# Kernel tuning notes

Hardware: AMD Instinct MI355X
Metric: run time of the kernel (lower is better)

Reference implementation:

```python
import jax, jax.numpy as jnp
import numpy as np

N = 1_000_000
F_IN = 16
HID = 32
E = 16_000_000


def setup_inputs() -> dict:
    key = jax.random.key(0)
    ks = jax.random.split(key, 20)
    s = 0.1
    inp = {
        "x": jax.random.normal(ks[0], (N, F_IN), dtype=jnp.float32),
        "edge_index": jax.random.randint(ks[1], (2, E), 0, N, dtype=jnp.int64),
        "edge_weight": jax.random.uniform(ks[2], (E,), dtype=jnp.float32),
        # ChebConv(K=1) weights for the 3 GRU gates (x-side and h-side)
        "Wxz": jax.random.normal(ks[3], (F_IN, HID), dtype=jnp.float32) * s,
        "bxz": jnp.zeros((HID,), jnp.float32),
        "Whz": jax.random.normal(ks[4], (HID, HID), dtype=jnp.float32) * s,
        "bhz": jnp.zeros((HID,), jnp.float32),
        "Wxr": jax.random.normal(ks[5], (F_IN, HID), dtype=jnp.float32) * s,
        "bxr": jnp.zeros((HID,), jnp.float32),
        "Whr": jax.random.normal(ks[6], (HID, HID), dtype=jnp.float32) * s,
        "bhr": jnp.zeros((HID,), jnp.float32),
        "Wxh": jax.random.normal(ks[7], (F_IN, HID), dtype=jnp.float32) * s,
        "bxh": jnp.zeros((HID,), jnp.float32),
        "Whh": jax.random.normal(ks[8], (HID, HID), dtype=jnp.float32) * s,
        "bhh": jnp.zeros((HID,), jnp.float32),
        # final Linear(32, 1)
        "Wlin": jax.random.normal(ks[9], (HID, 1), dtype=jnp.float32) * s,
        "blin": jnp.zeros((1,), jnp.float32),
    }
    return inp


def _gconv_gru(x, Wxz, bxz, Whz, bhz, Wxr, bxr, Whr, bhr, Wxh, bxh, Whh, bhh):
    # GConvGRU with ChebConv K=1: each conv is T0(L)x @ W + b == x @ W + b
    # (edge_index / edge_weight are mathematically unused when K=1).
    H = jnp.zeros((x.shape[0], Whz.shape[0]), dtype=x.dtype)  # initial hidden state
    Z = jax.nn.sigmoid(x @ Wxz + bxz + H @ Whz + bhz)          # update gate
    R = jax.nn.sigmoid(x @ Wxr + bxr + H @ Whr + bhr)          # reset gate
    H_tilde = jnp.tanh(x @ Wxh + bxh + (R * H) @ Whh + bhh)    # candidate
    return Z * H + (1.0 - Z) * H_tilde


def reference(x, edge_index, edge_weight, Wxz, bxz, Whz, bhz, Wxr, bxr, Whr, bhr,
              Wxh, bxh, Whh, bhh, Wlin, blin):
    H = _gconv_gru(x, Wxz, bxz, Whz, bhz, Wxr, bxr, Whr, bhr, Wxh, bxh, Whh, bhh)
    h = jax.nn.relu(H)
    return h @ Wlin + blin  # [N, 1]
```

## Files before the change

kernel.cpp:

```cpp
#include <hip/hip_runtime.h>


typedef float v2f __attribute__((ext_vector_type(2)));

constexpr int F   = 16;
constexpr int HD  = 32;
constexpr int NPT = 4;
constexpr int JB  = 4;

__global__ __launch_bounds__(256) void gru_fused(
    const float* __restrict__ x,
    const float* __restrict__ Wxz, const float* __restrict__ bxz,
    const float* __restrict__ bhz,
    const float* __restrict__ Wxh, const float* __restrict__ bxh,
    const float* __restrict__ bhh,
    const float* __restrict__ Wlin, const float* __restrict__ blin,
    float* __restrict__ out, int n)
{
    const int t = blockIdx.x * 256 + threadIdx.x;
    const int base = t * NPT;
    if (base >= n) return;

    float xs[NPT][F];
    #pragma unroll
    for (int m = 0; m < NPT; ++m) {
        const float4* xp = reinterpret_cast<const float4*>(x + (size_t)(base + m) * F);
        #pragma unroll
        for (int q = 0; q < 4; ++q) {
            float4 v = xp[q];
            xs[m][4 * q + 0] = v.x;
            xs[m][4 * q + 1] = v.y;
            xs[m][4 * q + 2] = v.z;
            xs[m][4 * q + 3] = v.w;
        }
    }

    float res[NPT];
    #pragma unroll
    for (int m = 0; m < NPT; ++m) res[m] = blin[0];

    #pragma unroll 1
    for (int jb = 0; jb < HD / JB; ++jb) {
        v2f accZ[JB][NPT / 2];
        v2f accH[JB][NPT / 2];
        #pragma unroll
        for (int j = 0; j < JB; ++j) {
            const int jj = jb * JB + j;
            const float bz = bxz[jj] + bhz[jj];
            const float bh = bxh[jj] + bhh[jj];
            #pragma unroll
            for (int p = 0; p < NPT / 2; ++p) {
                v2f vz = {bz, bz};
                v2f vh = {bh, bh};
                accZ[j][p] = vz;
                accH[j][p] = vh;
            }
        }

        #pragma unroll
        for (int k = 0; k < F; ++k) {
            v2f xk[NPT / 2];
            #pragma unroll
            for (int p = 0; p < NPT / 2; ++p) {
                v2f v = {xs[2 * p][k], xs[2 * p + 1][k]};
                xk[p] = v;
            }
            #pragma unroll
            for (int j = 0; j < JB; ++j) {
                const int jj = jb * JB + j;
                const float wz = Wxz[k * HD + jj];
                const float wh = Wxh[k * HD + jj];
                v2f wz2 = {wz, wz};
                v2f wh2 = {wh, wh};
                #pragma unroll
                for (int p = 0; p < NPT / 2; ++p) {
                    accZ[j][p] = __builtin_elementwise_fma(xk[p], wz2, accZ[j][p]);
                    accH[j][p] = __builtin_elementwise_fma(xk[p], wh2, accH[j][p]);
                }
            }
        }

        #pragma unroll
        for (int j = 0; j < JB; ++j) {
            const int jj = jb * JB + j;
            const float wl = Wlin[jj];
            #pragma unroll
            for (int p = 0; p < NPT / 2; ++p) {
                #pragma unroll
                for (int h = 0; h < 2; ++h) {
                    const float az = accZ[j][p][h];
                    const float ah = accH[j][p][h];
                    const float u = __expf(az);
                    const float v = __expf(fminf(2.f * ah, 87.f));
                    const float r = __builtin_amdgcn_rcpf((1.f + u) * (1.f + v));
                    const float num = fmaxf(v - 1.f, 0.f);
                    res[2 * p + h] = fmaf(num * r, wl, res[2 * p + h]);
                }
            }
        }
    }

    float4 o = make_float4(res[0], res[1], res[2], res[3]);
    *reinterpret_cast<float4*>(out + base) = o;
}

extern "C" void kernel_launch(void* const* d_in, const int* in_sizes, int n_in,
                              void* d_out, int out_size, void* d_ws, size_t ws_size,
                              hipStream_t stream) {
    const float* x    = (const float*)d_in[0];
    const float* Wxz  = (const float*)d_in[3];
    const float* bxz  = (const float*)d_in[4];
    const float* bhz  = (const float*)d_in[6];
    const float* Wxh  = (const float*)d_in[11];
    const float* bxh  = (const float*)d_in[12];
    const float* bhh  = (const float*)d_in[14];
    const float* Wlin = (const float*)d_in[15];
    const float* blin = (const float*)d_in[16];
    float* out = (float*)d_out;

    const int n = in_sizes[0] / F;
    const int threads = n / NPT;
    const int blocks = (threads + 255) / 256;
    gru_fused<<<blocks, 256, 0, stream>>>(
        x, Wxz, bxz, bhz, Wxh, bxh, bhh, Wlin, blin, out, n);
}
```

Baseline: 268.4 us.

## Halve nodes per thread and fully unroll hidden loop with occupancy hint

Each thread now handles 2 nodes instead of 4, packed as one v2f pair. The hidden dimension loop is fully unrolled over all 32 units rather than running as a rolled loop of 4-wide blocks, and __launch_bounds__ now requests 4 blocks per SM. The aim is lower register pressure, higher occupancy for this memory-bound kernel, and no loop overhead. In exchange, weight loads are amortised over fewer nodes per thread and twice as many threads are launched. The full unroll also grows code size.

```diff
diff --git a/kernel.cpp b/kernel.cpp
--- a/kernel.cpp
+++ b/kernel.cpp
@@ -5,10 +5,9 @@
 
 constexpr int F   = 16;
 constexpr int HD  = 32;
-constexpr int NPT = 4;
-constexpr int JB  = 4;
+constexpr int NPT = 2;
 
-__global__ __launch_bounds__(256) void gru_fused(
+__global__ __launch_bounds__(256, 4) void gru_fused(
     const float* __restrict__ x,
     const float* __restrict__ Wxz, const float* __restrict__ bxz,
     const float* __restrict__ bhz,
@@ -21,87 +20,53 @@
     const int base = t * NPT;
     if (base >= n) return;
 
-    float xs[NPT][F];
-    #pragma unroll
-    for (int m = 0; m < NPT; ++m) {
-        const float4* xp = reinterpret_cast<const float4*>(x + (size_t)(base + m) * F);
+    v2f xp[F];
+    {
+        float a[F], b[F];
+        const float4* p0 = reinterpret_cast<const float4*>(x + (size_t)base * F);
+        const float4* p1 = reinterpret_cast<const float4*>(x + (size_t)(base + 1) * F);
         #pragma unroll
         for (int q = 0; q < 4; ++q) {
-            float4 v = xp[q];
-            xs[m][4 * q + 0] = v.x;
-            xs[m][4 * q + 1] = v.y;
-            xs[m][4 * q + 2] = v.z;
-            xs[m][4 * q + 3] = v.w;
+            float4 v0 = p0[q], v1 = p1[q];
+            a[4*q+0]=v0.x; a[4*q+1]=v0.y; a[4*q+2]=v0.z; a[4*q+3]=v0.w;
+            b[4*q+0]=v1.x; b[4*q+1]=v1.y; b[4*q+2]=v1.z; b[4*q+3]=v1.w;
+        }
+        #pragma unroll
+        for (int k = 0; k < F; ++k) { v2f v = {a[k], b[k]}; xp[k] = v; }
+    }
+
+    v2f res = {blin[0], blin[0]};
+
+    #pragma unroll
+    for (int j = 0; j < HD; ++j) {
+        const float bz = bxz[j] + bhz[j];
+        const float bh = bxh[j] + bhh[j];
+        v2f aZ = {bz, bz};
+        v2f aH = {bh, bh};
+        #pragma unroll
+        for (int k = 0; k < F; ++k) {
+            const float wz = Wxz[k * HD + j];
+            const float wh = Wxh[k * HD + j];
+            v2f wz2 = {wz, wz};
+            v2f wh2 = {wh, wh};
+            aZ = __builtin_elementwise_fma(xp[k], wz2, aZ);
+            aH = __builtin_elementwise_fma(xp[k], wh2, aH);
+        }
+        const float wl = Wlin[j];
+        #pragma unroll
+        for (int h = 0; h < 2; ++h) {
+            const float az = aZ[h];
+            const float ah = aH[h];
+            const float u = __expf(az);
+            const float v = __expf(fminf(2.f * ah, 87.f));
+            const float r = __builtin_amdgcn_rcpf((1.f + u) * (1.f + v));
+            const float num = fmaxf(v - 1.f, 0.f);
+            res[h] = fmaf(num * r, wl, res[h]);
         }
     }
 
-    float res[NPT];
-    #pragma unroll
-    for (int m = 0; m < NPT; ++m) res[m] = blin[0];
-
-    #pragma unroll 1
-    for (int jb = 0; jb < HD / JB; ++jb) {
-        v2f accZ[JB][NPT / 2];
-        v2f accH[JB][NPT / 2];
-        #pragma unroll
-        for (int j = 0; j < JB; ++j) {
-            const int jj = jb * JB + j;
-            const float bz = bxz[jj] + bhz[jj];
-            const float bh = bxh[jj] + bhh[jj];
-            #pragma unroll
-            for (int p = 0; p < NPT / 2; ++p) {
-                v2f vz = {bz, bz};
-                v2f vh = {bh, bh};
-                accZ[j][p] = vz;
-                accH[j][p] = vh;
-            }
-        }
-
-        #pragma unroll
-        for (int k = 0; k < F; ++k) {
-            v2f xk[NPT / 2];
-            #pragma unroll
-            for (int p = 0; p < NPT / 2; ++p) {
-                v2f v = {xs[2 * p][k], xs[2 * p + 1][k]};
-                xk[p] = v;
-            }
-            #pragma unroll
-            for (int j = 0; j < JB; ++j) {
-                const int jj = jb * JB + j;
-                const float wz = Wxz[k * HD + jj];
-                const float wh = Wxh[k * HD + jj];
-                v2f wz2 = {wz, wz};
-                v2f wh2 = {wh, wh};
-                #pragma unroll
-                for (int p = 0; p < NPT / 2; ++p) {
-                    accZ[j][p] = __builtin_elementwise_fma(xk[p], wz2, accZ[j][p]);
-                    accH[j][p] = __builtin_elementwise_fma(xk[p], wh2, accH[j][p]);
-                }
-            }
-        }
-
-        #pragma unroll
-        for (int j = 0; j < JB; ++j) {
-            const int jj = jb * JB + j;
-            const float wl = Wlin[jj];
-            #pragma unroll
-            for (int p = 0; p < NPT / 2; ++p) {
-                #pragma unroll
-                for (int h = 0; h < 2; ++h) {
-                    const float az = accZ[j][p][h];
-                    const float ah = accH[j][p][h];
-                    const float u = __expf(az);
-                    const float v = __expf(fminf(2.f * ah, 87.f));
-                    const float r = __builtin_amdgcn_rcpf((1.f + u) * (1.f + v));
-                    const float num = fmaxf(v - 1.f, 0.f);
-                    res[2 * p + h] = fmaf(num * r, wl, res[2 * p + h]);
-                }
-            }
-        }
-    }
-
-    float4 o = make_float4(res[0], res[1], res[2], res[3]);
-    *reinterpret_cast<float4*>(out + base) = o;
+    float2 o = make_float2(res[0], res[1]);
+    *reinterpret_cast<float2*>(out + base) = o;
 }
 
 extern "C" void kernel_launch(void* const* d_in, const int* in_sizes, int n_in,
```

Result: slower. 485.8 us (+81.0%).
